# Kernel optimization log

Measured on AMD Instinct MI355X. Metric: run time of the kernel, lower is better.

The kernel has to match this reference:

```python
import jax, jax.numpy as jnp
import numpy as np

EPS = 1e-7
LN_EPS = 1e-5

# Lorentz model, points represented by spatial coords x in R^dim; time coord t = sqrt(K + ||x||^2), K = 1/c.

def log_map_zero(x, c):
    K = 1.0 / c
    sqrtK = jnp.sqrt(K)
    xnorm = jnp.linalg.norm(x, axis=-1, keepdims=True)
    t = jnp.sqrt(K + xnorm * xnorm)
    theta = jnp.arccosh(jnp.maximum(t / sqrtK, 1.0 + EPS))
    return sqrtK * theta * x / jnp.maximum(xnorm, EPS)


def exp_map_zero(v, c):
    K = 1.0 / c
    sqrtK = jnp.sqrt(K)
    vnorm = jnp.linalg.norm(v, axis=-1, keepdims=True)
    return sqrtK * jnp.sinh(vnorm / sqrtK) * v / jnp.maximum(vnorm, EPS)


def layer_norm(x, gamma, beta):
    mu = jnp.mean(x, axis=-1, keepdims=True)
    var = jnp.mean((x - mu) ** 2, axis=-1, keepdims=True)
    return (x - mu) * jax.lax.rsqrt(var + LN_EPS) * gamma + beta


def setup_inputs() -> dict:
    key = jax.random.key(0)
    N, D, E, L = 50000, 128, 800000, 2
    ks = jax.random.split(key, 8)
    x_hyp = jax.random.normal(ks[0], (N, D), dtype=jnp.float32)
    edge_index = jax.random.randint(ks[1], (2, E), 0, N, dtype=jnp.int64)
    W = jax.random.normal(ks[2], (L, D, D), dtype=jnp.float32) / np.sqrt(D)
    b = jnp.zeros((L, D), dtype=jnp.float32)
    gamma = jnp.ones((L, D), dtype=jnp.float32)
    beta = jnp.zeros((L, D), dtype=jnp.float32)
    curv = jnp.ones((L,), dtype=jnp.float32)
    return {"x_hyp": x_hyp, "edge_index": edge_index, "W": W, "b": b,
            "gamma": gamma, "beta": beta, "curv": curv}


def reference(x_hyp, edge_index, W, b, gamma, beta, curv):
    N = x_hyp.shape[0]
    L = W.shape[0]
    src, dst = edge_index[0], edge_index[1]
    # in-degree counts for mean aggregation (clamped to avoid div by 0)
    counts = jax.ops.segment_sum(jnp.ones_like(dst, dtype=x_hyp.dtype), dst, num_segments=N)
    counts = jnp.maximum(counts, 1.0)[:, None]
    x = x_hyp
    for l in range(L):
        # curvature treated as constant (torch uses .item())
        c = jax.lax.stop_gradient(jnp.clip(curv[l], 0.1, 10.0))
        x_tan = log_map_zero(x, c)                      # [N, D]
        x_lin = x_tan @ W[l].T + b[l]                   # [N, D]
        msgs = x_lin[src]                               # [E, D] gather
        agg = jax.ops.segment_sum(msgs, dst, num_segments=N) / counts  # scatter-mean
        x_tan_out = layer_norm(x_tan + agg, gamma[l], beta[l])  # dropout in eval mode
        x = exp_map_zero(x_tan_out, c)
    return x
```

## Files before the change

### kernel.cpp

```cpp
#include <hip/hip_runtime.h>
#include <hip/hip_bf16.h>

typedef __attribute__((ext_vector_type(4))) float f32x4;
typedef __attribute__((ext_vector_type(2))) float f32x2;
typedef __attribute__((ext_vector_type(8))) short bf16x8;

constexpr int D = 128;
constexpr int SB = 256;
constexpr int K4CAP = 8192;
#define FEPS 1e-7f
#define FLN_EPS 1e-5f

__device__ __forceinline__ float groupReduceSum16(float x) {
#pragma unroll
  for (int off = 1; off < 16; off <<= 1) x += __shfl_xor(x, off, 64);
  return x;
}

__device__ __forceinline__ unsigned short f2bf(float x) {
  unsigned int u = __float_as_uint(x);
  u += 0x7fffu + ((u >> 16) & 1u);
  return (unsigned short)(u >> 16);
}

__device__ __forceinline__ unsigned int pack2(float a, float b) {
  return (unsigned int)f2bf(a) | ((unsigned int)f2bf(b) << 16);
}

__device__ __forceinline__ f32x2 unp(unsigned int x) {
  f32x2 r;
  r.x = __uint_as_float(x << 16);
  r.y = __uint_as_float(x & 0xffff0000u);
  return r;
}

__device__ __forceinline__ void accp(f32x2* A, uint4 u) {
  A[0] += unp(u.x);
  A[1] += unp(u.y);
  A[2] += unp(u.z);
  A[3] += unp(u.w);
}


__global__ __launch_bounds__(1024) void k1_hist(const int* __restrict__ dst,
                                                int* __restrict__ bh, int E, int NB, int chunk) {
  __shared__ int h[256];
  int tid = threadIdx.x;
  if (tid < 256) h[tid] = 0;
  __syncthreads();
  int e0 = blockIdx.x * chunk;
  int e1 = min(e0 + chunk, E);
  for (int e = e0 + tid; e < e1; e += 1024) atomicAdd(&h[dst[e] >> 8], 1);
  __syncthreads();
  if (tid < NB) bh[tid * SB + blockIdx.x] = h[tid];
}

__global__ __launch_bounds__(1024) void k2_scan(int* __restrict__ bh,
                                                int* __restrict__ bucket_base, int NB, int E) {
  __shared__ int bsum[256];
  int tid = threadIdx.x, lane = tid & 63, wv = tid >> 6;
  for (int bin = wv; bin < NB; bin += 16) {
    int carry = 0;
    int* row = bh + bin * SB;
#pragma unroll
    for (int sgm = 0; sgm < 4; ++sgm) {
      int v = row[sgm * 64 + lane];
      int x = v;
#pragma unroll
      for (int off = 1; off < 64; off <<= 1) {
        int t = __shfl_up(x, off, 64);
        if (lane >= off) x += t;
      }
      row[sgm * 64 + lane] = carry + x - v;
      carry += __shfl(x, 63, 64);
    }
    if (lane == 0) bsum[bin] = carry;
  }
  __syncthreads();
  if (wv == 0) {
    int carry = 0;
    for (int base = 0; base < NB; base += 64) {
      int v = (base + lane < NB) ? bsum[base + lane] : 0;
      int x = v;
#pragma unroll
      for (int off = 1; off < 64; off <<= 1) {
        int t = __shfl_up(x, off, 64);
        if (lane >= off) x += t;
      }
      if (base + lane < NB) {
        int excl = carry + x - v;
        bsum[base + lane] = excl;
        bucket_base[base + lane] = excl;
      }
      carry += __shfl(x, 63, 64);
    }
    if (lane == 0) bucket_base[NB] = E;
  }
  __syncthreads();
  for (int bin = wv; bin < NB; bin += 16) {
    int bb = bsum[bin];
    int* row = bh + bin * SB;
    for (int s = lane; s < SB; s += 64) row[s] += bb;
  }
}

__global__ __launch_bounds__(1024) void k4_csr(const unsigned int* __restrict__ ebuf,
                                               const int* __restrict__ bucket_base,
                                               int* __restrict__ rowptr,
                                               unsigned short* __restrict__ col, int N, int NB,
                                               int E) {
  __shared__ unsigned int stash[K4CAP];
  __shared__ int hist[256];
  __shared__ int cur[256];
  int b = blockIdx.x, tid = threadIdx.x;
  int e0 = bucket_base[b], e1 = bucket_base[b + 1];
  int cnt = e1 - e0;
  if (tid < 256) {
    hist[tid] = 0;
    cur[tid] = 0;
  }
  __syncthreads();
  for (int i = tid; i < cnt; i += 1024) {
    unsigned int u = ebuf[e0 + i];
    if (i < K4CAP) stash[i] = u;
    atomicAdd(&hist[u >> 16], 1);
  }
  __syncthreads();
  int lane = tid & 63;
  if (tid < 64) {
    int carry = 0;
#pragma unroll
    for (int sgm = 0; sgm < 4; ++sgm) {
      int v = hist[sgm * 64 + lane];
      int x = v;
#pragma unroll
      for (int off = 1; off < 64; off <<= 1) {
        int t = __shfl_up(x, off, 64);
        if (lane >= off) x += t;
      }
      hist[sgm * 64 + lane] = carry + x - v;
      carry += __shfl(x, 63, 64);
    }
  }
  __syncthreads();
  int node0 = b << 8;
  if (tid < 256 && node0 + tid < N) rowptr[node0 + tid] = e0 + hist[tid];
  if (b == 0 && tid == 0) rowptr[N] = E;
  for (int i = tid; i < cnt; i += 1024) {
    unsigned int u = (i < K4CAP) ? stash[i] : ebuf[e0 + i];
    int slot = u >> 16;
    int r = atomicAdd(&cur[slot], 1);
    col[e0 + hist[slot] + r] = (unsigned short)(u & 0xffff);
  }
}


__global__ __launch_bounds__(1024) void bundle_kernel(
    const int* __restrict__ src, const int* __restrict__ dst, const int* __restrict__ bh,
    unsigned int* __restrict__ ebuf, int E, int NB, int chunk, const float* __restrict__ xf,
    const float* __restrict__ Wf, const float* __restrict__ curv,
    unsigned short* __restrict__ xt, int N, unsigned short* __restrict__ W16, int nconv,
    int lmblocks) {
  __shared__ int scratch[512];
  int bid = blockIdx.x;
  int tid = threadIdx.x;
  if (bid < SB) {
    int* base = scratch;
    int* cur = scratch + 256;
    if (tid < 256) {
      base[tid] = (tid < NB) ? bh[tid * SB + bid] : 0;
      cur[tid] = 0;
    }
    __syncthreads();
    int e0 = bid * chunk;
    int e1 = min(e0 + chunk, E);
    for (int e = e0 + tid; e < e1; e += 1024) {
      int d = dst[e];
      int s = src[e];
      int bin = d >> 8;
      int r = atomicAdd(&cur[bin], 1);
      ebuf[base[bin] + r] = (unsigned int)(s & 0xffff) | ((unsigned int)(d & 255) << 16);
    }
  } else if (bid < SB + lmblocks) {
    int lane = tid & 63, wv = tid >> 6;
    int gl = lane & 15, g = lane >> 4;
    int row = (bid - SB) * 64 + wv * 4 + g;
    bool active = row < N;
    int rd = active ? row : N - 1;
    float c = fminf(fmaxf(curv[0], 0.1f), 10.0f);
    float K = 1.0f / c, sqrtK = sqrtf(K);
    const float4* xr = reinterpret_cast<const float4*>(xf + (size_t)rd * D + gl * 8);
    float4 f0 = xr[0];
    float4 f1 = xr[1];
    float ss = f0.x * f0.x + f0.y * f0.y + f0.z * f0.z + f0.w * f0.w + f1.x * f1.x +
               f1.y * f1.y + f1.z * f1.z + f1.w * f1.w;
    ss = groupReduceSum16(ss);
    float xnorm = sqrtf(ss);
    float t = sqrtf(K + ss);
    float theta = acoshf(fmaxf(t / sqrtK, 1.0f + FEPS));
    float scale = sqrtK * theta / fmaxf(xnorm, FEPS);
    if (active) {
      uint4 w;
      w.x = pack2(f0.x * scale, f0.y * scale);
      w.y = pack2(f0.z * scale, f0.w * scale);
      w.z = pack2(f1.x * scale, f1.y * scale);
      w.w = pack2(f1.z * scale, f1.w * scale);
      reinterpret_cast<uint4*>(xt)[(size_t)row * 16 + gl] = w;
    }
  } else {
    for (int i = tid * 4; i < nconv; i += 4096) {
      float4 f = *reinterpret_cast<const float4*>(Wf + i);
      uint2 o;
      o.x = pack2(f.x, f.y);
      o.y = pack2(f.z, f.w);
      *reinterpret_cast<uint2*>(W16 + i) = o;
    }
  }
}


template <int MODE>
__global__ __launch_bounds__(256) void agg_kernel(const unsigned short* __restrict__ xt_in,
                                                  unsigned short* __restrict__ xt_out,
                                                  const int* __restrict__ rowptr,
                                                  const unsigned short* __restrict__ col,
                                                  const float* __restrict__ gamma,
                                                  const float* __restrict__ beta,
                                                  const float* __restrict__ curv, int l,
                                                  const unsigned short* __restrict__ Wl,
                                                  const float* __restrict__ bias,
                                                  float* __restrict__ out, int N) {
  __shared__ char smem[16 * 136 * 2 * 2];
  unsigned short* xhi = reinterpret_cast<unsigned short*>(smem);
  unsigned short* xlo = xhi + 16 * 136;
  float* ztile = reinterpret_cast<float*>(smem);
  int tid = threadIdx.x;
  int lane = tid & 63;
  int gl = lane & 15, g = lane >> 4;
  int wid = tid >> 6;
  int node = blockIdx.x * 16 + wid * 4 + g;
  bool active = node < N;
  int nd = active ? node : N - 1;

  float c = fminf(fmaxf(curv[l], 0.1f), 10.0f);
  float K = 1.0f / c, sqrtK = sqrtf(K);

  int e0 = rowptr[nd], e1 = rowptr[nd + 1];
  int deg = e1 - e0;
  const unsigned short* cb = col + e0;

  f32x2 A0[4], A1[4];
#pragma unroll
  for (int j = 0; j < 4; ++j) {
    A0[j] = 0.f;
    A1[j] = 0.f;
  }

  const uint4* xtp = reinterpret_cast<const uint4*>(xt_in);
  int cidx = (gl < deg) ? (int)cb[gl] : 0;
  for (int base = 0; base < deg; base += 16) {
    int nb = base + 16;
    int cnext = (nb + gl < deg) ? (int)cb[nb + gl] : 0;
    int m = deg - base;
    if (m > 16) m = 16;
    int k = 0;
    for (; k + 4 <= m; k += 4) {
      int s0 = __shfl(cidx, g * 16 + k, 64);
      int s1 = __shfl(cidx, g * 16 + k + 1, 64);
      int s2 = __shfl(cidx, g * 16 + k + 2, 64);
      int s3 = __shfl(cidx, g * 16 + k + 3, 64);
      uint4 u0 = xtp[(size_t)s0 * 16 + gl];
      uint4 u1 = xtp[(size_t)s1 * 16 + gl];
      uint4 u2 = xtp[(size_t)s2 * 16 + gl];
      uint4 u3 = xtp[(size_t)s3 * 16 + gl];
      accp(A0, u0);
      accp(A1, u1);
      accp(A0, u2);
      accp(A1, u3);
    }
    for (; k < m; ++k) {
      int s0 = __shfl(cidx, g * 16 + k, 64);
      uint4 u0 = xtp[(size_t)s0 * 16 + gl];
      accp(A0, u0);
    }
    cidx = cnext;
  }
  float a[8];
#pragma unroll
  for (int j = 0; j < 4; ++j) {
    f32x2 t = A0[j] + A1[j];
    a[2 * j] = t.x;
    a[2 * j + 1] = t.y;
  }

  float inv = 1.f / fmaxf((float)deg, 1.f);
  float flag = (deg > 0) ? 1.f : 0.f;

  int noderow = wid * 4 + g;
  {
    uint4 whi, wlo;
    unsigned int hb[8];
    float lo[8];
#pragma unroll
    for (int j = 0; j < 8; ++j) {
      float mj = a[j] * inv;
      unsigned short h = f2bf(mj);
      hb[j] = h;
      lo[j] = mj - __uint_as_float(((unsigned int)h) << 16);
    }
    whi.x = hb[0] | (hb[1] << 16);
    whi.y = hb[2] | (hb[3] << 16);
    whi.z = hb[4] | (hb[5] << 16);
    whi.w = hb[6] | (hb[7] << 16);
    wlo.x = pack2(lo[0], lo[1]);
    wlo.y = pack2(lo[2], lo[3]);
    wlo.z = pack2(lo[4], lo[5]);
    wlo.w = pack2(lo[6], lo[7]);
    *reinterpret_cast<uint4*>(&xhi[noderow * 136 + gl * 8]) = whi;
    *reinterpret_cast<uint4*>(&xlo[noderow * 136 + gl * 8]) = wlo;
  }
  __syncthreads();

  int rr = lane & 15, kg = lane >> 4;
  bf16x8 ah[4], al[4];
#pragma unroll
  for (int kb = 0; kb < 4; ++kb) {
    ah[kb] = *reinterpret_cast<const bf16x8*>(&xhi[rr * 136 + kb * 32 + kg * 8]);
    al[kb] = *reinterpret_cast<const bf16x8*>(&xlo[rr * 136 + kb * 32 + kg * 8]);
  }
  __syncthreads();

#pragma unroll
  for (int t = 0; t < 2; ++t) {
    int tcol = wid * 2 + t;
    f32x4 acc = {0.f, 0.f, 0.f, 0.f};
#pragma unroll
    for (int kb = 0; kb < 4; ++kb) {
      bf16x8 bfm = *reinterpret_cast<const bf16x8*>(Wl + (size_t)(tcol * 16 + rr) * D +
                                                    kb * 32 + kg * 8);
      acc = __builtin_amdgcn_mfma_f32_16x16x32_bf16(ah[kb], bfm, acc, 0, 0, 0);
      acc = __builtin_amdgcn_mfma_f32_16x16x32_bf16(al[kb], bfm, acc, 0, 0, 0);
    }
#pragma unroll
    for (int i = 0; i < 4; ++i) ztile[(kg * 4 + i) * 132 + tcol * 16 + rr] = acc[i];
  }
  __syncthreads();

  float4 wm0 = *reinterpret_cast<const float4*>(&ztile[noderow * 132 + gl * 8]);
  float4 wm1 = *reinterpret_cast<const float4*>(&ztile[noderow * 132 + gl * 8 + 4]);
  float4 bi0 = *reinterpret_cast<const float4*>(bias + l * D + gl * 8);
  float4 bi1 = *reinterpret_cast<const float4*>(bias + l * D + gl * 8 + 4);

  uint4 ut = xtp[(size_t)nd * 16 + gl];
  f32x2 utv[4];
  utv[0] = unp(ut.x);
  utv[1] = unp(ut.y);
  utv[2] = unp(ut.z);
  utv[3] = unp(ut.w);
  float v[8];
  v[0] = utv[0].x + wm0.x + bi0.x * flag;
  v[1] = utv[0].y + wm0.y + bi0.y * flag;
  v[2] = utv[1].x + wm0.z + bi0.z * flag;
  v[3] = utv[1].y + wm0.w + bi0.w * flag;
  v[4] = utv[2].x + wm1.x + bi1.x * flag;
  v[5] = utv[2].y + wm1.y + bi1.y * flag;
  v[6] = utv[3].x + wm1.z + bi1.z * flag;
  v[7] = utv[3].y + wm1.w + bi1.w * flag;

  float s1 = 0.f, s2 = 0.f;
#pragma unroll
  for (int j = 0; j < 8; ++j) {
    s1 += v[j];
    s2 += v[j] * v[j];
  }
  s1 = groupReduceSum16(s1);
  s2 = groupReduceSum16(s2);
  float mu = s1 * (1.f / 128.f);
  float var = fmaxf(s2 * (1.f / 128.f) - mu * mu, 0.f);
  float rstd = rsqrtf(var + FLN_EPS);

  float4 gm0 = *reinterpret_cast<const float4*>(gamma + l * D + gl * 8);
  float4 gm1 = *reinterpret_cast<const float4*>(gamma + l * D + gl * 8 + 4);
  float4 bt0 = *reinterpret_cast<const float4*>(beta + l * D + gl * 8);
  float4 bt1 = *reinterpret_cast<const float4*>(beta + l * D + gl * 8 + 4);
  float y[8];
  y[0] = (v[0] - mu) * rstd * gm0.x + bt0.x;
  y[1] = (v[1] - mu) * rstd * gm0.y + bt0.y;
  y[2] = (v[2] - mu) * rstd * gm0.z + bt0.z;
  y[3] = (v[3] - mu) * rstd * gm0.w + bt0.w;
  y[4] = (v[4] - mu) * rstd * gm1.x + bt1.x;
  y[5] = (v[5] - mu) * rstd * gm1.y + bt1.y;
  y[6] = (v[6] - mu) * rstd * gm1.z + bt1.z;
  y[7] = (v[7] - mu) * rstd * gm1.w + bt1.w;

  float ss = 0.f;
#pragma unroll
  for (int j = 0; j < 8; ++j) ss += y[j] * y[j];
  ss = groupReduceSum16(ss);
  float vn = sqrtf(ss);
  float sc = sqrtK * sinhf(vn / sqrtK) / fmaxf(vn, FEPS);

  if (MODE == 0) {
    if (active) {
      float4 o0, o1;
      o0.x = y[0] * sc;
      o0.y = y[1] * sc;
      o0.z = y[2] * sc;
      o0.w = y[3] * sc;
      o1.x = y[4] * sc;
      o1.y = y[5] * sc;
      o1.z = y[6] * sc;
      o1.w = y[7] * sc;
      float4* op = reinterpret_cast<float4*>(out + (size_t)node * D + gl * 8);
      op[0] = o0;
      op[1] = o1;
    }
  } else {
    float xn = sqrtK * sinhf(vn / sqrtK);
    float c2 = fminf(fmaxf(curv[l + 1], 0.1f), 10.0f);
    float K2 = 1.0f / c2, sqrtK2 = sqrtf(K2);
    float t2 = sqrtf(K2 + xn * xn);
    float theta = acoshf(fmaxf(t2 / sqrtK2, 1.0f + FEPS));
    float sc2 = sqrtK2 * theta / fmaxf(xn, FEPS);
    float st = sc * sc2;
    if (active) {
      uint4 w;
      w.x = pack2(y[0] * st, y[1] * st);
      w.y = pack2(y[2] * st, y[3] * st);
      w.z = pack2(y[4] * st, y[5] * st);
      w.w = pack2(y[6] * st, y[7] * st);
      reinterpret_cast<uint4*>(xt_out)[(size_t)node * 16 + gl] = w;
    }
  }
}


extern "C" void kernel_launch(void* const* d_in, const int* in_sizes, int n_in,
                              void* d_out, int out_size, void* d_ws, size_t ws_size,
                              hipStream_t stream) {
  const float* x_hyp = (const float*)d_in[0];
  const int* edge = (const int*)d_in[1];
  const float* W = (const float*)d_in[2];
  const float* b = (const float*)d_in[3];
  const float* gamma = (const float*)d_in[4];
  const float* beta = (const float*)d_in[5];
  const float* curv = (const float*)d_in[6];
  float* out = (float*)d_out;
  int N = in_sizes[0] / D;
  int E = in_sizes[1] / 2;
  int L = in_sizes[6];
  const int* src = edge;
  const int* dst = edge + E;

  char* p = (char*)d_ws;
  auto alloc = [&](size_t bytes) {
    char* r = p;
    p += (bytes + 255) & ~(size_t)255;
    return r;
  };
  int NB = (N + 255) >> 8;
  int chunk = (E + SB - 1) / SB;

  int* bh = (int*)alloc((size_t)256 * SB * 4);
  int* bucket_base = (int*)alloc((size_t)(NB + 1) * 4);
  unsigned int* ebuf = (unsigned int*)alloc((size_t)E * 4);
  int* rowptr = (int*)alloc((size_t)(N + 1) * 4);
  unsigned short* colp = (unsigned short*)alloc((size_t)E * 2);
  unsigned short* xtA = (unsigned short*)alloc((size_t)N * D * 2);
  unsigned short* xtB = (unsigned short*)alloc((size_t)N * D * 2);
  unsigned short* W16 = (unsigned short*)alloc((size_t)L * D * D * 2);

  int lmblocks = (N + 63) / 64;
  int nconv = L * D * D;

  k1_hist<<<SB, 1024, 0, stream>>>(dst, bh, E, NB, chunk);
  k2_scan<<<1, 1024, 0, stream>>>(bh, bucket_base, NB, E);
  bundle_kernel<<<SB + lmblocks + 1, 1024, 0, stream>>>(src, dst, bh, ebuf, E, NB, chunk,
                                                        x_hyp, W, curv, xtA, N, W16, nconv,
                                                        lmblocks);
  k4_csr<<<NB, 1024, 0, stream>>>(ebuf, bucket_base, rowptr, colp, N, NB, E);

  unsigned short* cur = xtA;
  unsigned short* nxt = xtB;
  for (int l = 0; l < L; ++l) {
    if (l < L - 1) {
      agg_kernel<1><<<(N + 15) / 16, 256, 0, stream>>>(cur, nxt, rowptr, colp, gamma, beta,
                                                       curv, l, W16 + (size_t)l * D * D, b,
                                                       out, N);
      unsigned short* tmp = cur;
      cur = nxt;
      nxt = tmp;
    } else {
      agg_kernel<0><<<(N + 15) / 16, 256, 0, stream>>>(cur, nullptr, rowptr, colp, gamma, beta,
                                                       curv, l, W16 + (size_t)l * D * D, b,
                                                       out, N);
    }
  }
}
```

Before: 145.4 us.

## Split gather-aggregation into feature-sliced kernel and separate epilogue kernel

The fused aggregate+GEMM+layernorm kernel becomes two kernels. A gather kernel splits each node's 128 features into 4 slices handled by separate blocks, with 4 lanes per node, and writes fp32 neighbor sums to a new buffer. The epilogue kernel then reads those sums and does the MFMA transform, layernorm and exp map. The aim is better cache locality (each block touches only a 64-byte slice of every row) and more parallelism in the gather. The cost is an extra kernel launch per layer and a full fp32 N×D round trip through global memory.

```diff
diff --git a/kernel.cpp b/kernel.cpp
--- a/kernel.cpp
+++ b/kernel.cpp
@@ -34,11 +34,24 @@
   return r;
 }
 
-__device__ __forceinline__ void accp(f32x2* A, uint4 u) {
-  A[0] += unp(u.x);
-  A[1] += unp(u.y);
-  A[2] += unp(u.z);
-  A[3] += unp(u.w);
+struct AccSet {
+  f32x2 e0, o0, e1, o1;
+};
+
+__device__ __forceinline__ void accu(AccSet& s, uint4 u) {
+  f32x2 t;
+  t.x = __uint_as_float(u.x << 16);
+  t.y = __uint_as_float(u.y << 16);
+  s.e0 += t;
+  t.x = __uint_as_float(u.x);
+  t.y = __uint_as_float(u.y);
+  s.o0 += t;
+  t.x = __uint_as_float(u.z << 16);
+  t.y = __uint_as_float(u.w << 16);
+  s.e1 += t;
+  t.x = __uint_as_float(u.z);
+  t.y = __uint_as_float(u.w);
+  s.o1 += t;
 }
 
 
@@ -219,11 +232,80 @@
 }
 
 
+__global__ __launch_bounds__(256) void gslice_kernel(const unsigned short* __restrict__ xt_in,
+                                                     const int* __restrict__ rowptr,
+                                                     const unsigned short* __restrict__ col,
+                                                     float* __restrict__ msum, int N) {
+  int bid = blockIdx.x;
+  int slice = bid & 3;
+  int chunk = bid >> 2;
+  int tid = threadIdx.x;
+  int lane = tid & 63, wv = tid >> 6;
+  int q = lane & 3;
+  int grp = lane >> 2;
+  int gbase = lane & ~3;
+  int node = chunk * 64 + wv * 16 + grp;
+  bool active = node < N;
+  int nd = active ? node : N - 1;
+
+  int e0 = rowptr[nd], e1 = rowptr[nd + 1];
+  int deg = e1 - e0;
+  const unsigned short* cb = col + e0;
+
+  AccSet S0, S1;
+  S0.e0 = 0.f; S0.o0 = 0.f; S0.e1 = 0.f; S0.o1 = 0.f;
+  S1.e0 = 0.f; S1.o0 = 0.f; S1.e1 = 0.f; S1.o1 = 0.f;
+
+  const uint4* xtp = reinterpret_cast<const uint4*>(xt_in);
+  int sb = slice * 4 + q;
+  int cidx = (q < deg) ? (int)cb[q] : 0;
+  for (int base = 0; base < deg; base += 4) {
+    int nb = base + 4;
+    int cnext = (nb + q < deg) ? (int)cb[nb + q] : 0;
+    int m = deg - base;
+    if (m > 4) m = 4;
+    if (m == 4) {
+      int s0 = __shfl(cidx, gbase, 64);
+      int s1 = __shfl(cidx, gbase + 1, 64);
+      int s2 = __shfl(cidx, gbase + 2, 64);
+      int s3 = __shfl(cidx, gbase + 3, 64);
+      uint4 u0 = xtp[(size_t)s0 * 16 + sb];
+      uint4 u1 = xtp[(size_t)s1 * 16 + sb];
+      uint4 u2 = xtp[(size_t)s2 * 16 + sb];
+      uint4 u3 = xtp[(size_t)s3 * 16 + sb];
+      accu(S0, u0);
+      accu(S1, u1);
+      accu(S0, u2);
+      accu(S1, u3);
+    } else {
+      for (int k = 0; k < m; ++k) {
+        int s0 = __shfl(cidx, gbase + k, 64);
+        accu(S0, xtp[(size_t)s0 * 16 + sb]);
+      }
+    }
+    cidx = cnext;
+  }
+  f32x2 E0 = S0.e0 + S1.e0;
+  f32x2 O0 = S0.o0 + S1.o0;
+  f32x2 E1 = S0.e1 + S1.e1;
+  f32x2 O1 = S0.o1 + S1.o1;
+
+  if (active) {
+    float4 w0, w1;
+    w0.x = E0.x; w0.y = O0.x; w0.z = E0.y; w0.w = O0.y;
+    w1.x = E1.x; w1.y = O1.x; w1.z = E1.y; w1.w = O1.y;
+    float4* mp = reinterpret_cast<float4*>(msum + (size_t)node * D + slice * 32 + q * 8);
+    mp[0] = w0;
+    mp[1] = w1;
+  }
+}
+
+
 template <int MODE>
-__global__ __launch_bounds__(256) void agg_kernel(const unsigned short* __restrict__ xt_in,
+__global__ __launch_bounds__(256) void epi_kernel(const unsigned short* __restrict__ xt_in,
                                                   unsigned short* __restrict__ xt_out,
+                                                  const float* __restrict__ msum,
                                                   const int* __restrict__ rowptr,
-                                                  const unsigned short* __restrict__ col,
                                                   const float* __restrict__ gamma,
                                                   const float* __restrict__ beta,
                                                   const float* __restrict__ curv, int l,
@@ -245,56 +327,14 @@
   float c = fminf(fmaxf(curv[l], 0.1f), 10.0f);
   float K = 1.0f / c, sqrtK = sqrtf(K);
 
-  int e0 = rowptr[nd], e1 = rowptr[nd + 1];
-  int deg = e1 - e0;
-  const unsigned short* cb = col + e0;
-
-  f32x2 A0[4], A1[4];
-#pragma unroll
-  for (int j = 0; j < 4; ++j) {
-    A0[j] = 0.f;
-    A1[j] = 0.f;
-  }
-
-  const uint4* xtp = reinterpret_cast<const uint4*>(xt_in);
-  int cidx = (gl < deg) ? (int)cb[gl] : 0;
-  for (int base = 0; base < deg; base += 16) {
-    int nb = base + 16;
-    int cnext = (nb + gl < deg) ? (int)cb[nb + gl] : 0;
-    int m = deg - base;
-    if (m > 16) m = 16;
-    int k = 0;
-    for (; k + 4 <= m; k += 4) {
-      int s0 = __shfl(cidx, g * 16 + k, 64);
-      int s1 = __shfl(cidx, g * 16 + k + 1, 64);
-      int s2 = __shfl(cidx, g * 16 + k + 2, 64);
-      int s3 = __shfl(cidx, g * 16 + k + 3, 64);
-      uint4 u0 = xtp[(size_t)s0 * 16 + gl];
-      uint4 u1 = xtp[(size_t)s1 * 16 + gl];
-      uint4 u2 = xtp[(size_t)s2 * 16 + gl];
-      uint4 u3 = xtp[(size_t)s3 * 16 + gl];
-      accp(A0, u0);
-      accp(A1, u1);
-      accp(A0, u2);
-      accp(A1, u3);
-    }
-    for (; k < m; ++k) {
-      int s0 = __shfl(cidx, g * 16 + k, 64);
-      uint4 u0 = xtp[(size_t)s0 * 16 + gl];
-      accp(A0, u0);
-    }
-    cidx = cnext;
-  }
-  float a[8];
-#pragma unroll
-  for (int j = 0; j < 4; ++j) {
-    f32x2 t = A0[j] + A1[j];
-    a[2 * j] = t.x;
-    a[2 * j + 1] = t.y;
-  }
-
+  int deg = rowptr[nd + 1] - rowptr[nd];
   float inv = 1.f / fmaxf((float)deg, 1.f);
   float flag = (deg > 0) ? 1.f : 0.f;
+
+  const float4* mp = reinterpret_cast<const float4*>(msum + (size_t)nd * D + gl * 8);
+  float4 ma = mp[0];
+  float4 mb = mp[1];
+  float a[8] = {ma.x, ma.y, ma.z, ma.w, mb.x, mb.y, mb.z, mb.w};
 
   int noderow = wid * 4 + g;
   {
@@ -351,6 +391,7 @@
   float4 bi0 = *reinterpret_cast<const float4*>(bias + l * D + gl * 8);
   float4 bi1 = *reinterpret_cast<const float4*>(bias + l * D + gl * 8 + 4);
 
+  const uint4* xtp = reinterpret_cast<const uint4*>(xt_in);
   uint4 ut = xtp[(size_t)nd * 16 + gl];
   f32x2 utv[4];
   utv[0] = unp(ut.x);
@@ -466,6 +507,7 @@
   unsigned int* ebuf = (unsigned int*)alloc((size_t)E * 4);
   int* rowptr = (int*)alloc((size_t)(N + 1) * 4);
   unsigned short* colp = (unsigned short*)alloc((size_t)E * 2);
+  float* msum = (float*)alloc((size_t)N * D * 4);
   unsigned short* xtA = (unsigned short*)alloc((size_t)N * D * 2);
   unsigned short* xtB = (unsigned short*)alloc((size_t)N * D * 2);
   unsigned short* W16 = (unsigned short*)alloc((size_t)L * D * D * 2);
@@ -480,20 +522,23 @@
                                                         lmblocks);
   k4_csr<<<NB, 1024, 0, stream>>>(ebuf, bucket_base, rowptr, colp, N, NB, E);
 
+  int gchunks = (N + 63) / 64;
+  int gblocks = gchunks * 4;
+  int eblocks = (N + 15) / 16;
+
   unsigned short* cur = xtA;
   unsigned short* nxt = xtB;
   for (int l = 0; l < L; ++l) {
+    gslice_kernel<<<gblocks, 256, 0, stream>>>(cur, rowptr, colp, msum, N);
     if (l < L - 1) {
-      agg_kernel<1><<<(N + 15) / 16, 256, 0, stream>>>(cur, nxt, rowptr, colp, gamma, beta,
-                                                       curv, l, W16 + (size_t)l * D * D, b,
-                                                       out, N);
+      epi_kernel<1><<<eblocks, 256, 0, stream>>>(cur, nxt, msum, rowptr, gamma, beta, curv, l,
+                                                 W16 + (size_t)l * D * D, b, out, N);
       unsigned short* tmp = cur;
       cur = nxt;
       nxt = tmp;
     } else {
-      agg_kernel<0><<<(N + 15) / 16, 256, 0, stream>>>(cur, nullptr, rowptr, colp, gamma, beta,
-                                                       curv, l, W16 + (size_t)l * D * D, b,
-                                                       out, N);
-    }
-  }
-}
+      epi_kernel<0><<<eblocks, 256, 0, stream>>>(cur, nullptr, msum, rowptr, gamma, beta, curv,
+                                                 l, W16 + (size_t)l * D * D, b, out, N);
+    }
+  }
+}
```

Result: slower. 196.3 us (+35.0%).
